# Kernel tuning notes

Hardware: AMD Instinct MI355X
Metric: run time of the kernel (lower is better)

Reference implementation:

```python
import jax, jax.numpy as jnp
import numpy as np

N_NODES = 100000
N_EDGES = 1600000
D_IN, D_HID, D_OUT = 128, 128, 64


def spmm(row, col, val, h, n):
    # y[i] = sum_{e: row[e]==i} val[e] * h[col[e]]  (A_hat @ h with A in COO form)
    return jax.ops.segment_sum(val[:, None] * h[col], row, num_segments=n)


def setup_inputs() -> dict:
    key = jax.random.key(0)
    ks = jax.random.split(key, 7)
    x = jax.random.normal(ks[0], (1, N_NODES, D_IN), dtype=jnp.float32)
    edge_row = jax.random.randint(ks[1], (N_EDGES,), 0, N_NODES, dtype=jnp.int32)
    edge_col = jax.random.randint(ks[2], (N_EDGES,), 0, N_NODES, dtype=jnp.int32)
    edge_val = jax.random.uniform(ks[3], (N_EDGES,), dtype=jnp.float32)
    W0 = jax.random.normal(ks[4], (D_HID, D_IN), dtype=jnp.float32) * 0.05
    W1 = jax.random.normal(ks[5], (D_HID, D_HID), dtype=jnp.float32) * 0.05
    W2 = jax.random.normal(ks[6], (D_OUT, D_HID), dtype=jnp.float32) * 0.05
    return {"x": x, "edge_row": edge_row, "edge_col": edge_col,
            "edge_val": edge_val, "W0": W0, "W1": W1, "W2": W2}


def reference(x, edge_row, edge_col, edge_val, W0, W1, W2):
    B, N, D = x.shape
    n = B * N
    h = x.reshape(n, D)
    # input conv: Linear (no bias) -> SpMM -> ReLU
    h = jax.nn.relu(spmm(edge_row, edge_col, edge_val, h @ W0.T, n))
    # hidden conv with residual: ReLU(A (h W1^T)) + h
    h = jax.nn.relu(spmm(edge_row, edge_col, edge_val, h @ W1.T, n)) + h
    # dropout is identity in eval mode
    out = spmm(edge_row, edge_col, edge_val, h @ W2.T, n)
    return out
```

## Files before the change

kernel.cpp:

```cpp
#include <hip/hip_runtime.h>


typedef unsigned int u32;
typedef unsigned short u16;
typedef __attribute__((ext_vector_type(8))) short bf16x8;
typedef __attribute__((ext_vector_type(4))) float f32x4;

constexpr int NN = 100000;
constexpr int NE = 1600000;
constexpr int PAD = 100352;
constexpr int NBUCK = 196;
constexpr int BCAP = 10240;
constexpr int EPB = 4096;
constexpr int P1B = (NE + EPB - 1) / EPB;
constexpr int G0B = (NN + 63) / 64;

__device__ __forceinline__ u16 f2bf(float f) {
    u32 x = __float_as_uint(f);
    x += 0x7fffu + ((x >> 16) & 1u);
    return (u16)(x >> 16);
}

__device__ __forceinline__ void wfrag_one(const float* __restrict__ W,
                                          u16* __restrict__ Wf, int total, int i)
{
    if (i < total) {
        const int j    = i & 7;
        const int lane = (i >> 3) & 63;
        const int kc   = (i >> 9) & 3;
        const int ct   = i >> 11;
        const int src  = (ct * 16 + (lane & 15)) * 128 + kc * 32 + (lane >> 4) * 8 + j;
        Wf[i] = f2bf(W[src]);
    }
}

__global__ __launch_bounds__(256)
void wcvt_kernel(const float* __restrict__ W0, const float* __restrict__ W1,
                 const float* __restrict__ W2, u16* __restrict__ wf0,
                 u16* __restrict__ wf1, u16* __restrict__ wf2,
                 int* __restrict__ bcur)
{
    const int i = blockIdx.x * 256 + threadIdx.x;
    if (blockIdx.x == 0) bcur[threadIdx.x] = 0;
    wfrag_one(W0, wf0, 128 * 128, i);
    wfrag_one(W1, wf1, 128 * 128, i);
    wfrag_one(W2, wf2, 64 * 128, i);
}

__global__ __launch_bounds__(256)
void k1_kernel(const float* __restrict__ x, const u16* __restrict__ Wf,
               u16* __restrict__ Cb,
               const int* __restrict__ erow, const int* __restrict__ ecol,
               const float* __restrict__ eval, int* __restrict__ bcur,
               int2* __restrict__ part)
{
    __shared__ u16 smem[64 * 136];
    const int tid = threadIdx.x;

    if ((int)blockIdx.x < P1B) {
        int* shist = (int*)smem;
        int* sbase = shist + NBUCK;
        for (int i = tid; i < NBUCK; i += 256) shist[i] = 0;
        __syncthreads();

        const int base = blockIdx.x * EPB;
        #pragma unroll
        for (int j = 0; j < EPB / 256; ++j) {
            const int e = base + j * 256 + tid;
            if (e < NE) atomicAdd(&shist[erow[e] >> 9], 1);
        }
        __syncthreads();
        for (int i = tid; i < NBUCK; i += 256) {
            const int c = shist[i];
            sbase[i] = c ? atomicAdd(&bcur[i], c) : 0;
            shist[i] = 0;
        }
        __syncthreads();
        #pragma unroll
        for (int j = 0; j < EPB / 256; ++j) {
            const int e = base + j * 256 + tid;
            if (e < NE) {
                const int r = erow[e];
                const int b = r >> 9;
                const int rk = atomicAdd(&shist[b], 1);
                part[b * BCAP + sbase[b] + rk] =
                    make_int2(((r & 511) << 17) | ecol[e], __float_as_int(eval[e]));
            }
        }
        return;
    }

    constexpr int RS   = 136;
    constexpr int PADW = 136;
    u16* sA = smem;
    u16* sC = smem;
    const int w    = tid >> 6;
    const int lane = tid & 63;
    const int m    = lane & 15;
    const int q    = lane >> 4;
    const int rowBase = ((int)blockIdx.x - P1B) * 64;

    #pragma unroll
    for (int i = 0; i < 8; ++i) {
        const int g = (i * 256 + tid) * 4;
        const int r = g >> 7, c = g & 127;
        float4 v = make_float4(0.f, 0.f, 0.f, 0.f);
        if (rowBase + r < NN) v = *(const float4*)(x + (size_t)(rowBase + r) * 128 + c);
        u16* d = &sA[r * RS + c];
        d[0] = f2bf(v.x); d[1] = f2bf(v.y); d[2] = f2bf(v.z); d[3] = f2bf(v.w);
    }
    __syncthreads();

    bf16x8 afrag[4];
    #pragma unroll
    for (int kc = 0; kc < 4; ++kc)
        afrag[kc] = *(const bf16x8*)&sA[(w * 16 + m) * RS + kc * 32 + q * 8];
    __syncthreads();

    #pragma unroll
    for (int ct = 0; ct < 8; ++ct) {
        f32x4 acc = {0.f, 0.f, 0.f, 0.f};
        #pragma unroll
        for (int kc = 0; kc < 4; ++kc) {
            const bf16x8 b = *(const bf16x8*)(Wf + (((ct * 4 + kc) * 64) + lane) * 8);
            acc = __builtin_amdgcn_mfma_f32_16x16x32_bf16(afrag[kc], b, acc, 0, 0, 0);
        }
        #pragma unroll
        for (int r = 0; r < 4; ++r)
            sC[(w * 16 + q * 4 + r) * PADW + ct * 16 + m] = f2bf(acc[r]);
    }
    __syncthreads();

    const int g    = lane >> 2;
    const int cb   = (lane & 3) * 32;
    const int grow = rowBase + w * 16 + g;
    if (grow < NN) {
        #pragma unroll
        for (int i = 0; i < 4; ++i) {
            const int4 v = *(const int4*)&sC[(w * 16 + g) * PADW + cb + i * 8];
            *(int4*)(Cb + (size_t)grow * 128 + cb + i * 8) = v;
        }
    }
}

__global__ __launch_bounds__(256)
void part2_kernel(const int* __restrict__ bcur, const int2* __restrict__ part,
                  int* __restrict__ offs, int2* __restrict__ pce)
{
    __shared__ int scnt[512];
    __shared__ int sdata[256];
    __shared__ int rowoff[512];
    const int b = blockIdx.x;
    const int tid = threadIdx.x;

    const int bv = (tid < NBUCK) ? bcur[tid] : 0;
    sdata[tid] = bv;
    __syncthreads();
    #pragma unroll
    for (int off = 1; off < 256; off <<= 1) {
        const int val = (tid >= off) ? sdata[tid - off] : 0;
        __syncthreads();
        sdata[tid] += val;
        __syncthreads();
    }
    const int gb = (b > 0) ? sdata[b - 1] : 0;
    const int cnt = bcur[b];
    __syncthreads();

    scnt[tid] = 0; scnt[tid + 256] = 0;
    __syncthreads();

    const int2* src = part + (size_t)b * BCAP;
    for (int i = tid; i < cnt; i += 256)
        atomicAdd(&scnt[((u32)src[i].x) >> 17], 1);
    __syncthreads();

    const int c0 = scnt[2 * tid];
    const int c1 = scnt[2 * tid + 1];
    const int tsum = c0 + c1;
    sdata[tid] = tsum;
    __syncthreads();
    #pragma unroll
    for (int off = 1; off < 256; off <<= 1) {
        const int val = (tid >= off) ? sdata[tid - off] : 0;
        __syncthreads();
        sdata[tid] += val;
        __syncthreads();
    }
    const int excl = sdata[tid] - tsum;
    rowoff[2 * tid]     = gb + excl;
    rowoff[2 * tid + 1] = gb + excl + c0;
    __syncthreads();

    offs[b * 512 + tid]       = rowoff[tid];
    offs[b * 512 + 256 + tid] = rowoff[tid + 256];
    __syncthreads();

    for (int i = tid; i < cnt; i += 256) {
        const int2 ev = src[i];
        const int rl = ((u32)ev.x) >> 17;
        const int pos = atomicAdd(&rowoff[rl], 1);
        pce[pos] = make_int2(ev.x & 0x1FFFF, ev.y);
    }
}

template<int LPC>
__device__ __forceinline__ void load_row(const u16* p, u32* u) {
    if constexpr (LPC == 8) {
        const uint4 t = *(const uint4*)p;
        u[0] = t.x; u[1] = t.y; u[2] = t.z; u[3] = t.w;
    } else {
        const uint2 t = *(const uint2*)p;
        u[0] = t.x; u[1] = t.y;
    }
}

template<int LPC>
__device__ __forceinline__ void fma_row(float v, const u32* u, float* a) {
    #pragma unroll
    for (int j = 0; j < LPC / 2; ++j) {
        a[2*j]   = fmaf(v, __uint_as_float(u[j] << 16),         a[2*j]);
        a[2*j+1] = fmaf(v, __uint_as_float(u[j] & 0xffff0000u), a[2*j+1]);
    }
}

template<int DO, int MODE>
__global__ __launch_bounds__(256)
void spmm_gemm(const int* __restrict__ offs, const int2* __restrict__ pce,
               const u16* __restrict__ Hb, const u16* __restrict__ Wf,
               const u16* __restrict__ Res, u16* __restrict__ Cb,
               u16* __restrict__ Hout)
{
    constexpr int RS   = 136;
    constexpr int PADW = DO + 8;
    __shared__ u16 smem[16 * 136];
    const int tid = threadIdx.x;
    const int ln  = tid & 15;
    const int rl  = tid >> 4;
    const int row = blockIdx.x * 16 + rl;

    const int s = offs[row];
    const int t = offs[row + 1];
    const u16* hbase = Hb + ln * 8;

    float a0[8], a1[8];
    #pragma unroll
    for (int j = 0; j < 8; ++j) { a0[j] = 0.f; a1[j] = 0.f; }

    int e = s;
    for (; e + 1 < t; e += 2) {
        const int2 e0 = pce[e];
        const int2 e1 = pce[e + 1];
        u32 u0[4], u1[4];
        load_row<8>(hbase + (size_t)e0.x * 128, u0);
        load_row<8>(hbase + (size_t)e1.x * 128, u1);
        fma_row<8>(__int_as_float(e0.y), u0, a0);
        fma_row<8>(__int_as_float(e1.y), u1, a1);
    }
    if (e < t) {
        const int2 e0 = pce[e];
        u32 u0[4];
        load_row<8>(hbase + (size_t)e0.x * 128, u0);
        fma_row<8>(__int_as_float(e0.y), u0, a0);
    }
    #pragma unroll
    for (int j = 0; j < 8; ++j) a0[j] = fmaxf(a0[j] + a1[j], 0.f);

    if constexpr (MODE == 2) {
        u32 r[4];
        load_row<8>(Res + (size_t)row * 128 + ln * 8, r);
        #pragma unroll
        for (int j = 0; j < 4; ++j) {
            a0[2*j]   += __uint_as_float(r[j] << 16);
            a0[2*j+1] += __uint_as_float(r[j] & 0xffff0000u);
        }
    }
    u32 o[4];
    #pragma unroll
    for (int j = 0; j < 4; ++j)
        o[j] = (u32)f2bf(a0[2*j]) | ((u32)f2bf(a0[2*j+1]) << 16);
    const uint4 packed = make_uint4(o[0], o[1], o[2], o[3]);
    *(uint4*)&smem[rl * RS + ln * 8] = packed;
    if constexpr (MODE == 1)
        *(uint4*)(Hout + (size_t)row * 128 + ln * 8) = packed;
    __syncthreads();

    constexpr int TPW = DO / 64;
    const int w    = tid >> 6;
    const int lane = tid & 63;
    const int m    = lane & 15;
    const int q    = lane >> 4;

    bf16x8 afrag[4];
    #pragma unroll
    for (int kc = 0; kc < 4; ++kc)
        afrag[kc] = *(const bf16x8*)&smem[m * RS + kc * 32 + q * 8];

    f32x4 acc[TPW];
    #pragma unroll
    for (int tw = 0; tw < TPW; ++tw) {
        const int ct = w * TPW + tw;
        acc[tw] = (f32x4){0.f, 0.f, 0.f, 0.f};
        #pragma unroll
        for (int kc = 0; kc < 4; ++kc) {
            const bf16x8 b = *(const bf16x8*)(Wf + (((ct * 4 + kc) * 64) + lane) * 8);
            acc[tw] = __builtin_amdgcn_mfma_f32_16x16x32_bf16(afrag[kc], b, acc[tw], 0, 0, 0);
        }
    }
    __syncthreads();

    #pragma unroll
    for (int tw = 0; tw < TPW; ++tw) {
        const int ct = w * TPW + tw;
        #pragma unroll
        for (int r = 0; r < 4; ++r)
            smem[(q * 4 + r) * PADW + ct * 16 + m] = f2bf(acc[tw][r]);
    }
    __syncthreads();

    if (DO == 128 || tid < 128) {
        const int g = tid * 8;
        const int r = g / DO;
        const int c = g % DO;
        const int4 v = *(const int4*)&smem[r * PADW + c];
        *(int4*)(Cb + ((size_t)blockIdx.x * 16 + r) * DO + c) = v;
    }
}

__global__ __launch_bounds__(256)
void spmm_out(const int* __restrict__ offs, const int2* __restrict__ pce,
              const u16* __restrict__ Hb, float* __restrict__ Y)
{
    const int ln  = threadIdx.x & 15;
    const int row = blockIdx.x * 16 + (threadIdx.x >> 4);
    if (row >= NN) return;
    const int s = offs[row];
    const int t = offs[row + 1];
    const u16* hbase = Hb + ln * 4;

    float a0[4], a1[4];
    #pragma unroll
    for (int j = 0; j < 4; ++j) { a0[j] = 0.f; a1[j] = 0.f; }

    int e = s;
    for (; e + 1 < t; e += 2) {
        const int2 e0 = pce[e];
        const int2 e1 = pce[e + 1];
        u32 u0[2], u1[2];
        load_row<4>(hbase + (size_t)e0.x * 64, u0);
        load_row<4>(hbase + (size_t)e1.x * 64, u1);
        fma_row<4>(__int_as_float(e0.y), u0, a0);
        fma_row<4>(__int_as_float(e1.y), u1, a1);
    }
    if (e < t) {
        const int2 e0 = pce[e];
        u32 u0[2];
        load_row<4>(hbase + (size_t)e0.x * 64, u0);
        fma_row<4>(__int_as_float(e0.y), u0, a0);
    }
    #pragma unroll
    for (int j = 0; j < 4; ++j) a0[j] += a1[j];
    *(float4*)(Y + (size_t)row * 64 + ln * 4) = make_float4(a0[0], a0[1], a0[2], a0[3]);
}

extern "C" void kernel_launch(void* const* d_in, const int* in_sizes, int n_in,
                              void* d_out, int out_size, void* d_ws, size_t ws_size,
                              hipStream_t stream) {
    const float* x    = (const float*)d_in[0];
    const int*   erow = (const int*)  d_in[1];
    const int*   ecol = (const int*)  d_in[2];
    const float* eval = (const float*)d_in[3];
    const float* W0   = (const float*)d_in[4];
    const float* W1   = (const float*)d_in[5];
    const float* W2   = (const float*)d_in[6];
    float* out = (float*)d_out;

    char* p = (char*)d_ws;
    const size_t BUFB = (size_t)NN * 128 * sizeof(u16);
    u16* t0b  = (u16*)p;  p += BUFB;
    u16* t1b  = (u16*)p;  p += BUFB;
    u16* h1b  = (u16*)p;  p += BUFB;
    u16* wf0  = (u16*)p;  p += 128 * 128 * 2;
    u16* wf1  = (u16*)p;  p += 128 * 128 * 2;
    u16* wf2  = (u16*)p;  p += 64 * 128 * 2;
    int* bcur   = (int*)p; p += 256 * 4;
    int* offs   = (int*)p; p += ((size_t)PAD + 256) * 4;
    int2* part  = (int2*)p; p += (size_t)NBUCK * BCAP * 8;
    int2* pce   = (int2*)p;

    const dim3 blk(256);
    const int rowBlocks = NN / 16;

    wcvt_kernel<<<64, blk, 0, stream>>>(W0, W1, W2, wf0, wf1, wf2, bcur);
    k1_kernel  <<<P1B + G0B, blk, 0, stream>>>(x, wf0, t0b, erow, ecol, eval, bcur, part);
    part2_kernel<<<NBUCK, blk, 0, stream>>>(bcur, part, offs, pce);
    spmm_gemm<128, 1><<<rowBlocks, blk, 0, stream>>>(offs, pce, t0b, wf1, nullptr, t1b, h1b);
    spmm_gemm<64, 2><<<rowBlocks, blk, 0, stream>>>(offs, pce, t1b, wf2, h1b, t0b, nullptr);
    spmm_out<<<rowBlocks, blk, 0, stream>>>(offs, pce, t0b, out);
}
```

Before: 357.1 us.

## Use finer row buckets and sort edges by column within rows in LDS

Halves the bucket size to 256 rows, which gives 392 buckets with a smaller capacity. Each part2 block now holds its edges in registers and scatters them into a shared-memory staging buffer over 13 column-range passes, so edges inside each row end up roughly ordered by column. It then writes the bucket out to global memory with coalesced stores instead of scattered ones. The intent is better gather locality in the later SpMM kernels and cheaper stores, at the cost of extra passes, a 36KB LDS buffer, and a fixed bucket capacity that could overflow.

```diff
diff --git a/kernel.cpp b/kernel.cpp
--- a/kernel.cpp
+++ b/kernel.cpp
@@ -9,11 +9,13 @@
 constexpr int NN = 100000;
 constexpr int NE = 1600000;
 constexpr int PAD = 100352;
-constexpr int NBUCK = 196;
-constexpr int BCAP = 10240;
+constexpr int NBUCK = 392;
+constexpr int BCAP = 4608;
 constexpr int EPB = 4096;
 constexpr int P1B = (NE + EPB - 1) / EPB;
 constexpr int G0B = (NN + 63) / 64;
+constexpr int EPT = BCAP / 256;
+constexpr int NPASS = 13;
 
 __device__ __forceinline__ u16 f2bf(float f) {
     u32 x = __float_as_uint(f);
@@ -41,7 +43,7 @@
                  int* __restrict__ bcur)
 {
     const int i = blockIdx.x * 256 + threadIdx.x;
-    if (blockIdx.x == 0) bcur[threadIdx.x] = 0;
+    if (i < 512) bcur[i] = 0;
     wfrag_one(W0, wf0, 128 * 128, i);
     wfrag_one(W1, wf1, 128 * 128, i);
     wfrag_one(W2, wf2, 64 * 128, i);
@@ -67,7 +69,7 @@
         #pragma unroll
         for (int j = 0; j < EPB / 256; ++j) {
             const int e = base + j * 256 + tid;
-            if (e < NE) atomicAdd(&shist[erow[e] >> 9], 1);
+            if (e < NE) atomicAdd(&shist[erow[e] >> 8], 1);
         }
         __syncthreads();
         for (int i = tid; i < NBUCK; i += 256) {
@@ -81,10 +83,10 @@
             const int e = base + j * 256 + tid;
             if (e < NE) {
                 const int r = erow[e];
-                const int b = r >> 9;
+                const int b = r >> 8;
                 const int rk = atomicAdd(&shist[b], 1);
-                part[b * BCAP + sbase[b] + rk] =
-                    make_int2(((r & 511) << 17) | ecol[e], __float_as_int(eval[e]));
+                part[(size_t)b * BCAP + sbase[b] + rk] =
+                    make_int2(((r & 255) << 17) | ecol[e], __float_as_int(eval[e]));
             }
         }
         return;
@@ -147,14 +149,44 @@
 void part2_kernel(const int* __restrict__ bcur, const int2* __restrict__ part,
                   int* __restrict__ offs, int2* __restrict__ pce)
 {
-    __shared__ int scnt[512];
+    __shared__ int scnt[256];
+    __shared__ int rowoff[256];
     __shared__ int sdata[256];
-    __shared__ int rowoff[512];
+    __shared__ int2 sout[BCAP];
     const int b = blockIdx.x;
     const int tid = threadIdx.x;
 
-    const int bv = (tid < NBUCK) ? bcur[tid] : 0;
-    sdata[tid] = bv;
+    const int cnt = bcur[b];
+    const int2* src = part + (size_t)b * BCAP;
+
+    int2 ed[EPT];
+    #pragma unroll
+    for (int j = 0; j < EPT; ++j) {
+        const int idx = j * 256 + tid;
+        ed[j] = (idx < cnt) ? src[idx] : make_int2(-1, 0);
+    }
+
+    int partial = 0;
+    for (int i = tid; i < b; i += 256) partial += bcur[i];
+    sdata[tid] = partial;
+    __syncthreads();
+    #pragma unroll
+    for (int off = 128; off > 0; off >>= 1) {
+        if (tid < off) sdata[tid] += sdata[tid + off];
+        __syncthreads();
+    }
+    const int gb = sdata[0];
+    __syncthreads();
+
+    scnt[tid] = 0;
+    __syncthreads();
+    #pragma unroll
+    for (int j = 0; j < EPT; ++j)
+        if (ed[j].x >= 0) atomicAdd(&scnt[((u32)ed[j].x) >> 17], 1);
+    __syncthreads();
+
+    const int c = scnt[tid];
+    sdata[tid] = c;
     __syncthreads();
     #pragma unroll
     for (int off = 1; off < 256; off <<= 1) {
@@ -163,44 +195,28 @@
         sdata[tid] += val;
         __syncthreads();
     }
-    const int gb = (b > 0) ? sdata[b - 1] : 0;
-    const int cnt = bcur[b];
-    __syncthreads();
-
-    scnt[tid] = 0; scnt[tid + 256] = 0;
-    __syncthreads();
-
-    const int2* src = part + (size_t)b * BCAP;
-    for (int i = tid; i < cnt; i += 256)
-        atomicAdd(&scnt[((u32)src[i].x) >> 17], 1);
-    __syncthreads();
-
-    const int c0 = scnt[2 * tid];
-    const int c1 = scnt[2 * tid + 1];
-    const int tsum = c0 + c1;
-    sdata[tid] = tsum;
-    __syncthreads();
-    #pragma unroll
-    for (int off = 1; off < 256; off <<= 1) {
-        const int val = (tid >= off) ? sdata[tid - off] : 0;
-        __syncthreads();
-        sdata[tid] += val;
-        __syncthreads();
-    }
-    const int excl = sdata[tid] - tsum;
-    rowoff[2 * tid]     = gb + excl;
-    rowoff[2 * tid + 1] = gb + excl + c0;
-    __syncthreads();
-
-    offs[b * 512 + tid]       = rowoff[tid];
-    offs[b * 512 + 256 + tid] = rowoff[tid + 256];
-    __syncthreads();
-
-    for (int i = tid; i < cnt; i += 256) {
-        const int2 ev = src[i];
-        const int rl = ((u32)ev.x) >> 17;
-        const int pos = atomicAdd(&rowoff[rl], 1);
-        pce[pos] = make_int2(ev.x & 0x1FFFF, ev.y);
+    const int excl = sdata[tid] - c;
+    rowoff[tid] = excl;
+    offs[b * 256 + tid] = gb + excl;
+    __syncthreads();
+
+    for (int p = 0; p < NPASS; ++p) {
+        #pragma unroll
+        for (int j = 0; j < EPT; ++j) {
+            const int key = ed[j].x & 0x1FFFF;
+            if ((key >> 13) == p) {
+                const int rl  = ((u32)ed[j].x) >> 17;
+                const int pos = atomicAdd(&rowoff[rl], 1);
+                sout[pos] = make_int2(key, ed[j].y);
+            }
+        }
+        __syncthreads();
+    }
+
+    #pragma unroll
+    for (int j = 0; j < EPT; ++j) {
+        const int idx = j * 256 + tid;
+        if (idx < cnt) pce[(size_t)gb + idx] = sout[idx];
     }
 }
 
@@ -383,7 +399,7 @@
     u16* wf0  = (u16*)p;  p += 128 * 128 * 2;
     u16* wf1  = (u16*)p;  p += 128 * 128 * 2;
     u16* wf2  = (u16*)p;  p += 64 * 128 * 2;
-    int* bcur   = (int*)p; p += 256 * 4;
+    int* bcur   = (int*)p; p += 512 * 4;
     int* offs   = (int*)p; p += ((size_t)PAD + 256) * 4;
     int2* part  = (int2*)p; p += (size_t)NBUCK * BCAP * 8;
     int2* pce   = (int2*)p;
```

New measurement: 357.3 us. Within noise of the previous version (+0.1%).
